# Optimization experiments

Measured on AMD Instinct MI355X. Metric: run time of the kernel, lower is better.

The kernel has to match this reference:

```python
import jax, jax.numpy as jnp
import numpy as np

D_MODEL = 1024
N_HEADS = 16
D_HEAD = D_MODEL // N_HEADS
D_FF = 4096
EPS = 1e-5
NEG = -1e10


def setup_inputs() -> dict:
    key = jax.random.key(0)
    ks = jax.random.split(key, 16)
    s = 0.02
    x = jax.random.normal(ks[0], (4, 1024, D_MODEL), dtype=jnp.float32)
    mask = jnp.ones((4, 1, 1, 1024), dtype=jnp.int32)
    return {
        "x": x,
        "mask": mask,
        "Wq": jax.random.normal(ks[1], (D_MODEL, D_MODEL), jnp.float32) * s,
        "Wk": jax.random.normal(ks[2], (D_MODEL, D_MODEL), jnp.float32) * s,
        "Wv": jax.random.normal(ks[3], (D_MODEL, D_MODEL), jnp.float32) * s,
        "Wp": jax.random.normal(ks[4], (D_MODEL, D_MODEL), jnp.float32) * s,
        "bp": jnp.zeros((D_MODEL,), jnp.float32),
        "W1": jax.random.normal(ks[5], (D_MODEL, D_FF), jnp.float32) * s,
        "b1": jnp.zeros((D_FF,), jnp.float32),
        "W2": jax.random.normal(ks[6], (D_FF, D_MODEL), jnp.float32) * s,
        "b2": jnp.zeros((D_MODEL,), jnp.float32),
        "g1": jnp.ones((D_MODEL,), jnp.float32),
        "be1": jnp.zeros((D_MODEL,), jnp.float32),
        "g2": jnp.ones((D_MODEL,), jnp.float32),
        "be2": jnp.zeros((D_MODEL,), jnp.float32),
    }


def _layer_norm(x, g, b):
    mu = jnp.mean(x, axis=-1, keepdims=True)
    var = jnp.mean(jnp.square(x - mu), axis=-1, keepdims=True)
    return (x - mu) * jax.lax.rsqrt(var + EPS) * g + b


def _mha(x, mask, Wq, Wk, Wv, Wp, bp):
    B, L, _ = x.shape
    q = (x @ Wq).reshape(B, L, N_HEADS, D_HEAD).transpose(0, 2, 1, 3)  # (B,H,L,dh)
    k = (x @ Wk).reshape(B, L, N_HEADS, D_HEAD).transpose(0, 2, 1, 3)
    v = (x @ Wv).reshape(B, L, N_HEADS, D_HEAD).transpose(0, 2, 1, 3)
    scores = jnp.einsum('bhqd,bhkd->bhqk', q, k) / jnp.sqrt(jnp.float32(D_HEAD))
    scores = jnp.where(mask == 0, NEG, scores)
    attn = jax.nn.softmax(scores, axis=-1)
    heads = jnp.einsum('bhqk,bhkd->bhqd', attn, v)  # (B,H,L,dh)
    heads = heads.transpose(0, 2, 1, 3).reshape(B, L, D_MODEL)
    return heads @ Wp + bp


def reference(x, mask, Wq, Wk, Wv, Wp, bp, W1, b1, W2, b2, g1, be1, g2, be2):
    # Post-norm residual sublayers (dropout inactive at inference)
    attn_out = _mha(x, mask, Wq, Wk, Wv, Wp, bp)
    h = _layer_norm(x + attn_out, g1, be1)
    ff = jax.nn.relu(h @ W1 + b1) @ W2 + b2
    out = _layer_norm(h + ff, g2, be2)
    return out
```

## Files before the change

### kernel.cpp

```cpp
#include <hip/hip_runtime.h>
#include <hip/hip_bf16.h>

typedef __attribute__((ext_vector_type(8))) short short8;
typedef __attribute__((ext_vector_type(4))) short short4v;
typedef __attribute__((ext_vector_type(4))) float float4v;

static __device__ __forceinline__ float b2f(short s) {
    return __builtin_bit_cast(float, ((unsigned)(unsigned short)s) << 16);
}
static __device__ __forceinline__ short f2b(float f) {
    unsigned x = __builtin_bit_cast(unsigned, f);
    unsigned r = (x + 0x7fffu + ((x >> 16) & 1u)) >> 16;
    return (short)r;
}
static __device__ __forceinline__ void gload_lds16(const short* g, short* l) {
    __builtin_amdgcn_global_load_lds(
        (const __attribute__((address_space(1))) void*)g,
        (__attribute__((address_space(3))) void*)l, 16, 0, 0);
}

__global__ __launch_bounds__(256) void cvt_k(const float* __restrict__ in,
                                             short* __restrict__ out)
{
    const size_t i = ((size_t)blockIdx.x * 256 + threadIdx.x) * 4;
    const float4v v = *(const float4v*)&in[i];
    short4v s;
#pragma unroll
    for (int j = 0; j < 4; j++) s[j] = f2b(v[j]);
    *(short4v*)&out[i] = s;
}

__global__ __launch_bounds__(256) void transpose_cvt_k(const float* __restrict__ in,
                                                       short* __restrict__ out,
                                                       int R, int C)
{
    __shared__ float tile[64][65];
    const int tx = threadIdx.x;
    const int r0 = blockIdx.y * 64, c0 = blockIdx.x * 64;
    const int lr = tx >> 4, lc = (tx & 15) * 4;
#pragma unroll
    for (int p = 0; p < 4; p++) {
        const float4v v = *(const float4v*)&in[(size_t)(r0 + lr + p * 16) * C + c0 + lc];
#pragma unroll
        for (int j = 0; j < 4; j++) tile[lr + p * 16][lc + j] = v[j];
    }
    __syncthreads();
    const int oc = tx >> 3, orr = (tx & 7) * 8;
#pragma unroll
    for (int p = 0; p < 2; p++) {
        const int c = oc + p * 32;
        short8 pk;
#pragma unroll
        for (int j = 0; j < 8; j++) pk[j] = f2b(tile[orr + j][c]);
        *(short8*)&out[(size_t)(c0 + c) * R + r0 + orr] = pk;
    }
}

template<int MODE, int BM, int BN, int KH>
__global__ __launch_bounds__(256) void gemm_bt(const short* __restrict__ X,
                                               const short* __restrict__ Wt,
                                               short* __restrict__ out,
                                               const float* __restrict__ bias,
                                               const short* __restrict__ res,
                                               int M, int N, int K)
{
    constexpr int MI = BM / 32, NI = BN / 32;
    __shared__ short As[KH][BM * 32];
    __shared__ short Bs[KH][BN * 32];
    const int tid = threadIdx.x;
    const int wave = tid >> 6, lane = tid & 63;
    const int quad = lane >> 4, l16 = lane & 15;

    int bx = blockIdx.x, by = blockIdx.y;
    {
        const int nbx = gridDim.x, nby = gridDim.y;
        if ((nby & 7) == 0) {
            const int g = by * nbx + bx;
            const int xcd = g & 7, local = g >> 3, Y = nby >> 3;
            by = xcd * Y + (local % Y);
            bx = local / Y;
        }
    }
    const int m0 = by * BM, n0 = bx * BN;
    const int wm = (wave >> 1) * (BM / 2), wn = (wave & 1) * (BN / 2);

    int kb = 0, ke = K;
    short* op = out;
    if (MODE == 5) {
        kb = blockIdx.z * (K >> 1);
        ke = kb + (K >> 1);
        op = out + (size_t)blockIdx.z * M * N;
    }

    const int srow = tid >> 2, sc8 = (tid & 3) * 8;

    float4v acc[MI][NI] = {};

    for (int k0 = kb; k0 < ke; k0 += KH * 32) {
#pragma unroll
        for (int c = 0; c < BM / 64; c++)
#pragma unroll
            for (int h = 0; h < KH; h++)
                gload_lds16(X + (size_t)(m0 + c * 64 + srow) * K + k0 + h * 32 + sc8,
                            &As[h][(c * 256 + tid) * 8]);
#pragma unroll
        for (int c = 0; c < BN / 64; c++)
#pragma unroll
            for (int h = 0; h < KH; h++)
                gload_lds16(Wt + (size_t)(n0 + c * 64 + srow) * K + k0 + h * 32 + sc8,
                            &Bs[h][(c * 256 + tid) * 8]);
        __syncthreads();
#pragma unroll
        for (int h = 0; h < KH; h++) {
            short8 af[MI], bf[NI];
#pragma unroll
            for (int i = 0; i < MI; i++) af[i] = *(const short8*)&As[h][(wm + i * 16 + l16) * 32 + quad * 8];
#pragma unroll
            for (int i = 0; i < NI; i++) bf[i] = *(const short8*)&Bs[h][(wn + i * 16 + l16) * 32 + quad * 8];
#pragma unroll
            for (int mi = 0; mi < MI; mi++)
#pragma unroll
                for (int ni = 0; ni < NI; ni++)
                    acc[mi][ni] = __builtin_amdgcn_mfma_f32_16x16x32_bf16(af[mi], bf[ni], acc[mi][ni], 0, 0, 0);
        }
        __syncthreads();
    }

#pragma unroll
    for (int mi = 0; mi < MI; mi++) {
#pragma unroll
        for (int ni = 0; ni < NI; ni++) {
            const int gn = n0 + wn + ni * 16 + l16;
            const float bv = (MODE == 2 || MODE == 3) ? bias[gn] : 0.0f;
#pragma unroll
            for (int r = 0; r < 4; r++) {
                const int gm = m0 + wm + mi * 16 + quad * 4 + r;
                float v = acc[mi][ni][r];
                if (MODE == 4) {
                    const int s = gn >> 10;
                    const int n = gn & 1023;
                    const int hh = n >> 6, d = n & 63;
                    const size_t bh16 = (size_t)((gm >> 10) * 16 + hh) << 16;
                    const size_t base = (size_t)s << 22;
                    if (s == 0)      out[base + bh16 + ((size_t)(gm & 1023) << 6) + d] = f2b(v * 0.125f);
                    else if (s == 1) out[base + bh16 + ((size_t)(gm & 1023) << 6) + d] = f2b(v);
                    else             out[base + bh16 + ((size_t)d << 10) + (gm & 1023)] = f2b(v);
                } else if (MODE == 2) {
                    v += bv;
                    v = fmaxf(v, 0.0f);
                    out[(size_t)gm * N + gn] = f2b(v);
                } else if (MODE == 5) {
                    op[(size_t)gm * N + gn] = f2b(v);
                } else {
                    v += bv + b2f(res[(size_t)gm * N + gn]);
                    out[(size_t)gm * N + gn] = f2b(v);
                }
            }
        }
    }
}

__global__ __launch_bounds__(256) void sk_red_k(const short* __restrict__ p0,
                                                const short* __restrict__ p1,
                                                const float* __restrict__ bias,
                                                const short* __restrict__ res,
                                                short* __restrict__ out)
{
    const size_t i = ((size_t)blockIdx.x * 256 + threadIdx.x) * 4;
    const short4v a = *(const short4v*)&p0[i];
    const short4v b = *(const short4v*)&p1[i];
    const short4v c = *(const short4v*)&res[i];
    const float4v bv = *(const float4v*)&bias[i & 1023];
    short4v w;
#pragma unroll
    for (int j = 0; j < 4; j++) w[j] = f2b(b2f(a[j]) + b2f(b[j]) + bv[j] + b2f(c[j]));
    *(short4v*)&out[i] = w;
}

__global__ __launch_bounds__(256) void attn_k(const short* __restrict__ Qb,
                                              const short* __restrict__ Kb,
                                              const short* __restrict__ Vt,
                                              const int* __restrict__ mask,
                                              short* __restrict__ heads)
{
    __shared__ short Kl[2][64 * 32];
    __shared__ short Vl[2][64 * 32];
    __shared__ short P[4][16 * 72];
    const int bh = blockIdx.x, qb = blockIdx.y;
    const int b = bh >> 4, h = bh & 15;
    const int tid = threadIdx.x, wave = tid >> 6, lane = tid & 63;
    const int quad = lane >> 4, l16 = lane & 15;
    const int qbase = qb * 64 + wave * 16;
    const short* Qp = Qb + ((size_t)bh << 16) + (size_t)qbase * 64;
    const short* Kp = Kb + ((size_t)bh << 16);
    const short* Vp = Vt + ((size_t)bh << 16);
    const int* mp = mask + (b << 10);

    const short8 bq0 = *(const short8*)&Qp[l16 * 64 + quad * 8];
    const short8 bq1 = *(const short8*)&Qp[l16 * 64 + 32 + quad * 8];

    float rs = 0.0f;
    float4v o[4] = {};
    short* myP = &P[wave][0];

    const int srow = tid >> 2, sc8 = (tid & 3) * 8;

    for (int kc = 0; kc < 1024; kc += 64) {
        gload_lds16(Kp + (size_t)(kc + srow) * 64 + sc8,      &Kl[0][tid * 8]);
        gload_lds16(Kp + (size_t)(kc + srow) * 64 + 32 + sc8, &Kl[1][tid * 8]);
        gload_lds16(Vp + (size_t)srow * 1024 + kc + sc8,      &Vl[0][tid * 8]);
        gload_lds16(Vp + (size_t)srow * 1024 + kc + 32 + sc8, &Vl[1][tid * 8]);
        __syncthreads();

        float4v s[4];
#pragma unroll
        for (int kt = 0; kt < 4; kt++) {
            s[kt] = (float4v){};
            const short8 ka = *(const short8*)&Kl[0][(kt * 16 + l16) * 32 + quad * 8];
            s[kt] = __builtin_amdgcn_mfma_f32_16x16x32_bf16(ka, bq0, s[kt], 0, 0, 0);
            const short8 kb = *(const short8*)&Kl[1][(kt * 16 + l16) * 32 + quad * 8];
            s[kt] = __builtin_amdgcn_mfma_f32_16x16x32_bf16(kb, bq1, s[kt], 0, 0, 0);
        }
#pragma unroll
        for (int kt = 0; kt < 4; kt++) {
            const int4 mv = *(const int4*)&mp[kc + kt * 16 + quad * 4];
            float p0 = mv.x ? __expf(fminf(s[kt][0], 30.f)) : 0.f;
            float p1 = mv.y ? __expf(fminf(s[kt][1], 30.f)) : 0.f;
            float p2 = mv.z ? __expf(fminf(s[kt][2], 30.f)) : 0.f;
            float p3 = mv.w ? __expf(fminf(s[kt][3], 30.f)) : 0.f;
            rs += (p0 + p1) + (p2 + p3);
            short4v w;
            w[0] = f2b(p0); w[1] = f2b(p1); w[2] = f2b(p2); w[3] = f2b(p3);
            *(short4v*)&myP[l16 * 72 + kt * 16 + quad * 4] = w;
        }
        const short8 bp0 = *(const short8*)&myP[l16 * 72 + quad * 8];
        const short8 bp1 = *(const short8*)&myP[l16 * 72 + 32 + quad * 8];
#pragma unroll
        for (int dt = 0; dt < 4; dt++) {
            const short8 va = *(const short8*)&Vl[0][(dt * 16 + l16) * 32 + quad * 8];
            o[dt] = __builtin_amdgcn_mfma_f32_16x16x32_bf16(va, bp0, o[dt], 0, 0, 0);
            const short8 vb = *(const short8*)&Vl[1][(dt * 16 + l16) * 32 + quad * 8];
            o[dt] = __builtin_amdgcn_mfma_f32_16x16x32_bf16(vb, bp1, o[dt], 0, 0, 0);
        }
        __syncthreads();
    }

    rs += __shfl_xor(rs, 16);
    rs += __shfl_xor(rs, 32);
    const float inv = 1.0f / fmaxf(rs, 1e-20f);
    const int gq = qbase + l16;
#pragma unroll
    for (int dt = 0; dt < 4; dt++) {
        short4v w;
#pragma unroll
        for (int r = 0; r < 4; r++) w[r] = f2b(o[dt][r] * inv);
        *(short4v*)&heads[((size_t)(b * 1024 + gq) << 10) + h * 64 + dt * 16 + quad * 4] = w;
    }
}

template<bool F32OUT>
__global__ __launch_bounds__(256) void ln_k(const short* __restrict__ in,
                                            const float* __restrict__ g,
                                            const float* __restrict__ be,
                                            short* __restrict__ outb,
                                            float* __restrict__ outf)
{
    __shared__ float red[8];
    const int row = blockIdx.x, tid = threadIdx.x;
    const short* p = in + ((size_t)row << 10);
    float v[4];
#pragma unroll
    for (int i = 0; i < 4; i++) v[i] = b2f(p[tid + i * 256]);
    float s = v[0] + v[1] + v[2] + v[3];
#pragma unroll
    for (int off = 32; off; off >>= 1) s += __shfl_xor(s, off);
    if ((tid & 63) == 0) red[tid >> 6] = s;
    __syncthreads();
    const float mu = (red[0] + red[1] + red[2] + red[3]) * (1.0f / 1024.0f);
    float vs = 0.f;
#pragma unroll
    for (int i = 0; i < 4; i++) { const float d = v[i] - mu; vs += d * d; }
#pragma unroll
    for (int off = 32; off; off >>= 1) vs += __shfl_xor(vs, off);
    if ((tid & 63) == 0) red[4 + (tid >> 6)] = vs;
    __syncthreads();
    const float rstd = rsqrtf((red[4] + red[5] + red[6] + red[7]) * (1.0f / 1024.0f) + 1e-5f);
#pragma unroll
    for (int i = 0; i < 4; i++) {
        const int c = tid + i * 256;
        const float r = (v[i] - mu) * rstd * g[c] + be[c];
        if (F32OUT) outf[((size_t)row << 10) + c] = r;
        else        outb[((size_t)row << 10) + c] = f2b(r);
    }
}

extern "C" void kernel_launch(void* const* d_in, const int* in_sizes, int n_in,
                              void* d_out, int out_size, void* d_ws, size_t ws_size,
                              hipStream_t stream)
{
    const float* x   = (const float*)d_in[0];
    const int*   mk  = (const int*)d_in[1];
    const float* Wq  = (const float*)d_in[2];
    const float* Wk  = (const float*)d_in[3];
    const float* Wv  = (const float*)d_in[4];
    const float* Wp  = (const float*)d_in[5];
    const float* bp  = (const float*)d_in[6];
    const float* W1  = (const float*)d_in[7];
    const float* b1  = (const float*)d_in[8];
    const float* W2  = (const float*)d_in[9];
    const float* b2  = (const float*)d_in[10];
    const float* g1  = (const float*)d_in[11];
    const float* be1 = (const float*)d_in[12];
    const float* g2  = (const float*)d_in[13];
    const float* be2 = (const float*)d_in[14];
    float* out = (float*)d_out;

    char* ws = (char*)d_ws;
    const size_t MB = (size_t)1 << 20;
    short* xb     = (short*)(ws + 0 * MB);
    short* WqkvT  = (short*)(ws + 8 * MB);
    short* WpT    = (short*)(ws + 14 * MB);
    short* W1T    = (short*)(ws + 16 * MB);
    short* W2T    = (short*)(ws + 24 * MB);
    short* Qb     = (short*)(ws + 32 * MB);
    short* Kb     = (short*)(ws + 40 * MB);
    short* Vt     = (short*)(ws + 48 * MB);
    short* hd     = (short*)(ws + 56 * MB);
    short* u      = (short*)(ws + 32 * MB);
    short* hpre   = (short*)(ws + 64 * MB);
    short* hbuf   = (short*)(ws + 72 * MB);
    short* part   = (short*)(ws + 0 * MB);

    const dim3 blk(256);

    cvt_k<<<dim3(4096), blk, 0, stream>>>(x, xb);

    transpose_cvt_k<<<dim3(16, 16), blk, 0, stream>>>(Wq, WqkvT, 1024, 1024);
    transpose_cvt_k<<<dim3(16, 16), blk, 0, stream>>>(Wk, WqkvT + (1 << 20), 1024, 1024);
    transpose_cvt_k<<<dim3(16, 16), blk, 0, stream>>>(Wv, WqkvT + (2 << 20), 1024, 1024);
    transpose_cvt_k<<<dim3(16, 16), blk, 0, stream>>>(Wp, WpT, 1024, 1024);
    transpose_cvt_k<<<dim3(64, 16), blk, 0, stream>>>(W1, W1T, 1024, 4096);
    transpose_cvt_k<<<dim3(16, 64), blk, 0, stream>>>(W2, W2T, 4096, 1024);

    gemm_bt<4, 128, 128, 2><<<dim3(24, 32), blk, 0, stream>>>(xb, WqkvT, Qb, nullptr, nullptr, 4096, 3072, 1024);

    attn_k<<<dim3(64, 16), blk, 0, stream>>>(Qb, Kb, Vt, mk, hd);

    gemm_bt<3, 64, 64, 4><<<dim3(16, 64), blk, 0, stream>>>(hd, WpT, hpre, bp, xb, 4096, 1024, 1024);

    ln_k<false><<<dim3(4096), blk, 0, stream>>>(hpre, g1, be1, hbuf, nullptr);

    gemm_bt<2, 128, 128, 2><<<dim3(32, 32), blk, 0, stream>>>(hbuf, W1T, u, b1, nullptr, 4096, 4096, 1024);

    gemm_bt<5, 128, 128, 2><<<dim3(8, 32, 2), blk, 0, stream>>>(u, W2T, part, nullptr, nullptr, 4096, 1024, 4096);

    sk_red_k<<<dim3(4096), blk, 0, stream>>>(part, part + (4u << 20), b2, hbuf, hpre);

    ln_k<true><<<dim3(4096), blk, 0, stream>>>(hpre, g2, be2, nullptr, out);
}
```

Before: 346.1 us.

## Merge prep kernels, split-K the output projection, fuse reduction with layernorm

The six conversion/transpose launches are merged into one prep kernel that picks its job from the block index. The Wp projection moves from a 64x64 tile with a fused residual epilogue to a 128x128 split-K (two halves) GEMM writing bf16 partials. The split-K reduction, bias and residual add are fused into the layernorm kernel for both sublayers, which also switches to vectorized row loads. This drops several launches and intermediate round trips but adds partial-buffer traffic and an extra bf16 rounding of the partials for the projection.

Measured after the change: 338.0 us. 2.3% less time.

```diff
diff --git a/kernel.cpp b/kernel.cpp
--- a/kernel.cpp
+++ b/kernel.cpp
@@ -19,24 +19,13 @@
         (__attribute__((address_space(3))) void*)l, 16, 0, 0);
 }
 
-__global__ __launch_bounds__(256) void cvt_k(const float* __restrict__ in,
-                                             short* __restrict__ out)
-{
-    const size_t i = ((size_t)blockIdx.x * 256 + threadIdx.x) * 4;
-    const float4v v = *(const float4v*)&in[i];
-    short4v s;
-#pragma unroll
-    for (int j = 0; j < 4; j++) s[j] = f2b(v[j]);
-    *(short4v*)&out[i] = s;
-}
-
-__global__ __launch_bounds__(256) void transpose_cvt_k(const float* __restrict__ in,
-                                                       short* __restrict__ out,
-                                                       int R, int C)
-{
-    __shared__ float tile[64][65];
+static __device__ __forceinline__ void tile_transpose(const float* __restrict__ in,
+                                                      short* __restrict__ out,
+                                                      int R, int C, int bx, int by,
+                                                      float tile[64][65])
+{
     const int tx = threadIdx.x;
-    const int r0 = blockIdx.y * 64, c0 = blockIdx.x * 64;
+    const int r0 = by * 64, c0 = bx * 64;
     const int lr = tx >> 4, lc = (tx & 15) * 4;
 #pragma unroll
     for (int p = 0; p < 4; p++) {
@@ -53,6 +42,43 @@
 #pragma unroll
         for (int j = 0; j < 8; j++) pk[j] = f2b(tile[orr + j][c]);
         *(short8*)&out[(size_t)(c0 + c) * R + r0 + orr] = pk;
+    }
+}
+
+__global__ __launch_bounds__(256) void prep_k(const float* __restrict__ x,
+                                              const float* __restrict__ Wq,
+                                              const float* __restrict__ Wk,
+                                              const float* __restrict__ Wv,
+                                              const float* __restrict__ Wp,
+                                              const float* __restrict__ W1,
+                                              const float* __restrict__ W2,
+                                              short* __restrict__ xb,
+                                              short* __restrict__ WqkvT,
+                                              short* __restrict__ WpT,
+                                              short* __restrict__ W1T,
+                                              short* __restrict__ W2T)
+{
+    __shared__ float tile[64][65];
+    const int b = blockIdx.x;
+    if (b < 4096) {
+        const size_t i = ((size_t)b * 256 + threadIdx.x) * 4;
+        const float4v v = *(const float4v*)&x[i];
+        short4v s;
+#pragma unroll
+        for (int j = 0; j < 4; j++) s[j] = f2b(v[j]);
+        *(short4v*)&xb[i] = s;
+    } else if (b < 5120) {
+        const int lb = b - 4096;
+        const int wsel = lb >> 8, t = lb & 255;
+        const float* in = (wsel == 0) ? Wq : (wsel == 1) ? Wk : (wsel == 2) ? Wv : Wp;
+        short* out = (wsel < 3) ? (WqkvT + ((size_t)wsel << 20)) : WpT;
+        tile_transpose(in, out, 1024, 1024, t & 15, t >> 4, tile);
+    } else if (b < 6144) {
+        const int lb = b - 5120;
+        tile_transpose(W1, W1T, 1024, 4096, lb & 63, lb >> 6, tile);
+    } else {
+        const int lb = b - 6144;
+        tile_transpose(W2, W2T, 4096, 1024, lb & 15, lb >> 4, tile);
     }
 }
 
@@ -131,7 +157,7 @@
 #pragma unroll
         for (int ni = 0; ni < NI; ni++) {
             const int gn = n0 + wn + ni * 16 + l16;
-            const float bv = (MODE == 2 || MODE == 3) ? bias[gn] : 0.0f;
+            const float bv = (MODE == 2) ? bias[gn] : 0.0f;
 #pragma unroll
             for (int r = 0; r < 4; r++) {
                 const int gm = m0 + wm + mi * 16 + quad * 4 + r;
@@ -149,32 +175,12 @@
                     v += bv;
                     v = fmaxf(v, 0.0f);
                     out[(size_t)gm * N + gn] = f2b(v);
-                } else if (MODE == 5) {
+                } else {
                     op[(size_t)gm * N + gn] = f2b(v);
-                } else {
-                    v += bv + b2f(res[(size_t)gm * N + gn]);
-                    out[(size_t)gm * N + gn] = f2b(v);
                 }
             }
         }
     }
-}
-
-__global__ __launch_bounds__(256) void sk_red_k(const short* __restrict__ p0,
-                                                const short* __restrict__ p1,
-                                                const float* __restrict__ bias,
-                                                const short* __restrict__ res,
-                                                short* __restrict__ out)
-{
-    const size_t i = ((size_t)blockIdx.x * 256 + threadIdx.x) * 4;
-    const short4v a = *(const short4v*)&p0[i];
-    const short4v b = *(const short4v*)&p1[i];
-    const short4v c = *(const short4v*)&res[i];
-    const float4v bv = *(const float4v*)&bias[i & 1023];
-    short4v w;
-#pragma unroll
-    for (int j = 0; j < 4; j++) w[j] = f2b(b2f(a[j]) + b2f(b[j]) + bv[j] + b2f(c[j]));
-    *(short4v*)&out[i] = w;
 }
 
 __global__ __launch_bounds__(256) void attn_k(const short* __restrict__ Qb,
@@ -259,18 +265,25 @@
 }
 
 template<bool F32OUT>
-__global__ __launch_bounds__(256) void ln_k(const short* __restrict__ in,
-                                            const float* __restrict__ g,
-                                            const float* __restrict__ be,
-                                            short* __restrict__ outb,
-                                            float* __restrict__ outf)
+__global__ __launch_bounds__(256) void red_ln_k(const short* __restrict__ p0,
+                                                const short* __restrict__ p1,
+                                                const float* __restrict__ bias,
+                                                const short* __restrict__ res,
+                                                const float* __restrict__ g,
+                                                const float* __restrict__ be,
+                                                short* __restrict__ outb,
+                                                float* __restrict__ outf)
 {
     __shared__ float red[8];
     const int row = blockIdx.x, tid = threadIdx.x;
-    const short* p = in + ((size_t)row << 10);
+    const size_t base = ((size_t)row << 10) + tid * 4;
+    const short4v a = *(const short4v*)&p0[base];
+    const short4v b = *(const short4v*)&p1[base];
+    const short4v c = *(const short4v*)&res[base];
+    const float4v bv = *(const float4v*)&bias[tid * 4];
     float v[4];
 #pragma unroll
-    for (int i = 0; i < 4; i++) v[i] = b2f(p[tid + i * 256]);
+    for (int i = 0; i < 4; i++) v[i] = b2f(a[i]) + b2f(b[i]) + bv[i] + b2f(c[i]);
     float s = v[0] + v[1] + v[2] + v[3];
 #pragma unroll
     for (int off = 32; off; off >>= 1) s += __shfl_xor(s, off);
@@ -285,12 +298,18 @@
     if ((tid & 63) == 0) red[4 + (tid >> 6)] = vs;
     __syncthreads();
     const float rstd = rsqrtf((red[4] + red[5] + red[6] + red[7]) * (1.0f / 1024.0f) + 1e-5f);
-#pragma unroll
-    for (int i = 0; i < 4; i++) {
-        const int c = tid + i * 256;
-        const float r = (v[i] - mu) * rstd * g[c] + be[c];
-        if (F32OUT) outf[((size_t)row << 10) + c] = r;
-        else        outb[((size_t)row << 10) + c] = f2b(r);
+    const float4v gv = *(const float4v*)&g[tid * 4];
+    const float4v bev = *(const float4v*)&be[tid * 4];
+    if (F32OUT) {
+        float4v w;
+#pragma unroll
+        for (int i = 0; i < 4; i++) w[i] = (v[i] - mu) * rstd * gv[i] + bev[i];
+        *(float4v*)&outf[base] = w;
+    } else {
+        short4v w;
+#pragma unroll
+        for (int i = 0; i < 4; i++) w[i] = f2b((v[i] - mu) * rstd * gv[i] + bev[i]);
+        *(short4v*)&outb[base] = w;
     }
 }
 
@@ -326,35 +345,27 @@
     short* Kb     = (short*)(ws + 40 * MB);
     short* Vt     = (short*)(ws + 48 * MB);
     short* hd     = (short*)(ws + 56 * MB);
+    short* partP  = (short*)(ws + 32 * MB);
     short* u      = (short*)(ws + 32 * MB);
-    short* hpre   = (short*)(ws + 64 * MB);
+    short* partF  = (short*)(ws + 0 * MB);
     short* hbuf   = (short*)(ws + 72 * MB);
-    short* part   = (short*)(ws + 0 * MB);
 
     const dim3 blk(256);
 
-    cvt_k<<<dim3(4096), blk, 0, stream>>>(x, xb);
-
-    transpose_cvt_k<<<dim3(16, 16), blk, 0, stream>>>(Wq, WqkvT, 1024, 1024);
-    transpose_cvt_k<<<dim3(16, 16), blk, 0, stream>>>(Wk, WqkvT + (1 << 20), 1024, 1024);
-    transpose_cvt_k<<<dim3(16, 16), blk, 0, stream>>>(Wv, WqkvT + (2 << 20), 1024, 1024);
-    transpose_cvt_k<<<dim3(16, 16), blk, 0, stream>>>(Wp, WpT, 1024, 1024);
-    transpose_cvt_k<<<dim3(64, 16), blk, 0, stream>>>(W1, W1T, 1024, 4096);
-    transpose_cvt_k<<<dim3(16, 64), blk, 0, stream>>>(W2, W2T, 4096, 1024);
+    prep_k<<<dim3(7168), blk, 0, stream>>>(x, Wq, Wk, Wv, Wp, W1, W2,
+                                           xb, WqkvT, WpT, W1T, W2T);
 
     gemm_bt<4, 128, 128, 2><<<dim3(24, 32), blk, 0, stream>>>(xb, WqkvT, Qb, nullptr, nullptr, 4096, 3072, 1024);
 
     attn_k<<<dim3(64, 16), blk, 0, stream>>>(Qb, Kb, Vt, mk, hd);
 
-    gemm_bt<3, 64, 64, 4><<<dim3(16, 64), blk, 0, stream>>>(hd, WpT, hpre, bp, xb, 4096, 1024, 1024);
-
-    ln_k<false><<<dim3(4096), blk, 0, stream>>>(hpre, g1, be1, hbuf, nullptr);
+    gemm_bt<5, 128, 128, 2><<<dim3(8, 32, 2), blk, 0, stream>>>(hd, WpT, partP, nullptr, nullptr, 4096, 1024, 1024);
+
+    red_ln_k<false><<<dim3(4096), blk, 0, stream>>>(partP, partP + (4u << 20), bp, xb, g1, be1, hbuf, nullptr);
 
     gemm_bt<2, 128, 128, 2><<<dim3(32, 32), blk, 0, stream>>>(hbuf, W1T, u, b1, nullptr, 4096, 4096, 1024);
 
-    gemm_bt<5, 128, 128, 2><<<dim3(8, 32, 2), blk, 0, stream>>>(u, W2T, part, nullptr, nullptr, 4096, 1024, 4096);
-
-    sk_red_k<<<dim3(4096), blk, 0, stream>>>(part, part + (4u << 20), b2, hbuf, hpre);
-
-    ln_k<true><<<dim3(4096), blk, 0, stream>>>(hpre, g2, be2, nullptr, out);
-}
+    gemm_bt<5, 128, 128, 2><<<dim3(8, 32, 2), blk, 0, stream>>>(u, W2T, partF, nullptr, nullptr, 4096, 1024, 4096);
+
+    red_ln_k<true><<<dim3(4096), blk, 0, stream>>>(partF, partF + (4u << 20), b2, hbuf, g2, be2, nullptr, out);
+}
```
